# Kernel optimization log

Measured on AMD Instinct MI355X. Metric: run time of the kernel, lower is better.

## Reference

```python
import jax, jax.numpy as jnp
import numpy as np

B, S, D_IN, HID, H, OUT = 4, 2048, 1024, 1024, 16, 128
DH = HID // H
SCALE = float(np.sqrt(DH))
ELEV, FLOOR2 = 4, 32


def setup_inputs() -> dict:
    key = jax.random.key(0)
    ks = jax.random.split(key, 12)
    w = lambda k, o, i: jax.random.normal(k, (o, i), dtype=jnp.float32) * 0.02
    b = lambda k, o: jax.random.normal(k, (o,), dtype=jnp.float32) * 0.02
    return {
        "query": jax.random.normal(ks[0], (B, S, D_IN), dtype=jnp.float32),
        "key": jax.random.normal(ks[1], (B, S, D_IN), dtype=jnp.float32),
        "value": jax.random.normal(ks[2], (B, S, D_IN), dtype=jnp.float32),
        "mask": jax.random.randint(ks[3], (B, 1, 1, S), 0, 2, dtype=jnp.int32),
        "wq_w": w(ks[4], HID, D_IN), "wq_b": b(ks[5], HID),
        "wk_w": w(ks[6], HID, D_IN), "wk_b": b(ks[7], HID),
        "wv_w": w(ks[8], HID, D_IN), "wv_b": b(ks[9], HID),
        "fc_w": w(ks[10], OUT, HID), "fc_b": b(ks[11], OUT),
    }


def reference(query, key, value, mask, wq_w, wq_b, wk_w, wk_b, wv_w, wv_b, fc_w, fc_b):
    bsz, seq = query.shape[0], query.shape[1]
    # torch Linear: x @ W.T + b
    split = lambda x: x.reshape(bsz, seq, H, DH).transpose(0, 2, 1, 3)  # (b,h,s,dh)
    Q = split(query @ wq_w.T + wq_b)
    K = split(key @ wk_w.T + wk_b)
    V = split(value @ wv_w.T + wv_b)
    energy = jnp.einsum('bhqd,bhkd->bhqk', Q, K) / SCALE
    energy = jnp.where(mask == 0, jnp.float32(-1e10), energy)
    attn = jax.nn.softmax(energy, axis=-1)  # dropout is identity in eval mode
    x = jnp.einsum('bhqk,bhkd->bhqd', attn, V)
    x = x.transpose(0, 2, 1, 3).reshape(bsz, seq, HID)
    x = x @ fc_w.T + fc_b
    x = x.reshape(-1, ELEV, FLOOR2)  # (b*s, elevator_num, floor_num*2)
    return jax.nn.softmax(x, axis=1)  # nn.Softmax(dim=1)
```

## Files before the change

### kernel.cpp

```cpp
#include <hip/hip_runtime.h>
#include <stdint.h>

#define S_LEN 2048
#define DK 1024
#define NH 16
#define DH 64
#define LOG2E 1.4426950408889634f
#define M_FIX 10.0f

typedef __attribute__((ext_vector_type(8))) short bf16x8;
typedef __attribute__((ext_vector_type(4))) float f32x4;

__device__ __forceinline__ unsigned short f2bf(float f) {
    union { float f; uint32_t u; } v; v.f = f;
    return (unsigned short)((v.u + 0x7fffu + ((v.u >> 16) & 1u)) >> 16);
}

__device__ __forceinline__ float fast_exp2(float x) {
#if __has_builtin(__builtin_amdgcn_exp2f)
    return __builtin_amdgcn_exp2f(x);
#else
    return exp2f(x);
#endif
}

__device__ __forceinline__ uint32_t cvt_pk_bf16(float a, float b) {
    uint32_t r;
    asm("v_cvt_pk_bf16_f32 %0, %1, %2" : "=v"(r) : "v"(a), "v"(b));
    return r;
}

__device__ __forceinline__ void gload_lds16(const void* g, void* l) {
    __builtin_amdgcn_global_load_lds((const __attribute__((address_space(1))) void*)g,
                                     (__attribute__((address_space(3))) void*)l, 16, 0, 0);
}

__global__ __launch_bounds__(256) void cvt7_kernel(
    const float* __restrict__ a0, const float* __restrict__ a1, const float* __restrict__ a2,
    const float* __restrict__ a3, const float* __restrict__ a4, const float* __restrict__ a5,
    const float* __restrict__ a6,
    unsigned short* __restrict__ o0, unsigned short* __restrict__ o1, unsigned short* __restrict__ o2,
    unsigned short* __restrict__ o3, unsigned short* __restrict__ o4, unsigned short* __restrict__ o5,
    unsigned short* __restrict__ o6,
    int n4_big, int n4_w, int n4_f)
{
    const int y = blockIdx.y;
    const float* in = (y == 0) ? a0 : (y == 1) ? a1 : (y == 2) ? a2 :
                      (y == 3) ? a3 : (y == 4) ? a4 : (y == 5) ? a5 : a6;
    unsigned short* out = (y == 0) ? o0 : (y == 1) ? o1 : (y == 2) ? o2 :
                          (y == 3) ? o3 : (y == 4) ? o4 : (y == 5) ? o5 : o6;
    const int n4 = (y < 3) ? n4_big : ((y < 6) ? n4_w : n4_f);
    const float4* pin = (const float4*)in;
    ushort4* pout = (ushort4*)out;
    int i = blockIdx.x * blockDim.x + threadIdx.x;
    int stride = gridDim.x * blockDim.x;
    for (; i < n4; i += stride) {
        float4 v = pin[i];
        ushort4 o;
        o.x = f2bf(v.x); o.y = f2bf(v.y); o.z = f2bf(v.z); o.w = f2bf(v.w);
        pout[i] = o;
    }
}

__global__ __launch_bounds__(512) void proj_gemm(
    const unsigned short* __restrict__ Xq, const unsigned short* __restrict__ Xk, const unsigned short* __restrict__ Xv,
    const unsigned short* __restrict__ Wq, const unsigned short* __restrict__ Wk, const unsigned short* __restrict__ Wv,
    const float* __restrict__ bq, const float* __restrict__ bk, const float* __restrict__ bv,
    unsigned short* __restrict__ Qh, unsigned short* __restrict__ Kh, unsigned short* __restrict__ Vt)
{
    const int d = blockIdx.x + (blockIdx.y << 3) + (blockIdx.z << 9);
    const int k = d & 7, s = d >> 3;
    const int nn = s & 7;
    const int mz = ((s >> 3) << 3) + k;
    const int m0 = (mz & 63) * 128;
    const int z = mz >> 6;

    const unsigned short* X = (z == 0) ? Xq : ((z == 1) ? Xk : Xv);
    const unsigned short* W = (z == 0) ? Wq : ((z == 1) ? Wk : Wv);
    const float* bias = (z == 0) ? bq : ((z == 1) ? bk : bv);

    const int n0 = nn * 128;
    const int tid = threadIdx.x;
    const int w = tid >> 6;
    const int l = tid & 63;
    const int wm = w >> 2, wn = w & 3;
    const int g = l >> 4, c = l & 15;

    __shared__ __align__(16) unsigned short As[3][128 * 32];
    __shared__ __align__(16) unsigned short Bs[3][128 * 32];

    f32x4 acc[4][2] = {};

    const int srow = l >> 2;
    const int schunk = (((l & 3) - (l >> 3)) & 3) * 8;

    auto stage = [&](int kk, int buf) {
        int r0 = 16 * w;
        gload_lds16(X + (size_t)(m0 + r0 + srow) * DK + kk + schunk, &As[buf][r0 * 32]);
        gload_lds16(W + (size_t)(n0 + r0 + srow) * DK + kk + schunk, &Bs[buf][r0 * 32]);
    };

    stage(0, 0);
    stage(32, 1);

    int cur = 0;
    for (int step = 0; step < 32; ++step) {
        if (step < 31) asm volatile("s_waitcnt vmcnt(2)" ::: "memory");
        else           asm volatile("s_waitcnt vmcnt(0)" ::: "memory");
        __builtin_amdgcn_s_barrier();
        __builtin_amdgcn_sched_barrier(0);

        if (step < 30) {
            int nb = cur + 2; if (nb >= 3) nb -= 3;
            stage((step + 2) << 5, nb);
        }

        bf16x8 a[4], bb[2];
        const int rchunk = 8 * ((g + (c >> 1)) & 3);
#pragma unroll
        for (int mi = 0; mi < 4; ++mi)
            a[mi] = *(const bf16x8*)&As[cur][(64 * wm + 16 * mi + c) * 32 + rchunk];
#pragma unroll
        for (int nj = 0; nj < 2; ++nj)
            bb[nj] = *(const bf16x8*)&Bs[cur][(32 * wn + 16 * nj + c) * 32 + rchunk];
        __builtin_amdgcn_s_setprio(1);
#pragma unroll
        for (int mi = 0; mi < 4; ++mi)
#pragma unroll
            for (int nj = 0; nj < 2; ++nj)
                acc[mi][nj] = __builtin_amdgcn_mfma_f32_16x16x32_bf16(a[mi], bb[nj], acc[mi][nj], 0, 0, 0);
        __builtin_amdgcn_s_setprio(0);

        ++cur; if (cur == 3) cur = 0;
    }

    const float scale = (z == 0) ? (0.125f * LOG2E) : 1.0f;
#pragma unroll
    for (int mi = 0; mi < 4; ++mi) {
#pragma unroll
        for (int nj = 0; nj < 2; ++nj) {
            int col = n0 + 32 * wn + 16 * nj + c;
            float bval = bias[col];
            int h = col >> 6, dh = col & 63;
            int row0 = m0 + 64 * wm + 16 * mi + 4 * g;
            int b = row0 >> 11, ss = row0 & 2047;
            if (z != 2) {
                unsigned short* Out = (z == 0) ? Qh : Kh;
#pragma unroll
                for (int r = 0; r < 4; ++r) {
                    float v = (acc[mi][nj][r] + bval) * scale;
                    Out[((size_t)(b * NH + h) * S_LEN + (ss + r)) * DH + dh] = f2bf(v);
                }
            } else {
                ushort4 o;
                o.x = f2bf(acc[mi][nj][0] + bval);
                o.y = f2bf(acc[mi][nj][1] + bval);
                o.z = f2bf(acc[mi][nj][2] + bval);
                o.w = f2bf(acc[mi][nj][3] + bval);
                int q = (ss >> 2) & 7;
                int newpos = (ss & ~31) + 8 * (q & 3) + 4 * (q >> 2);
                *(ushort4*)&Vt[((size_t)(b * NH + h) * DH + dh) * S_LEN + newpos] = o;
            }
        }
    }
}

__global__ __launch_bounds__(256, 4) void attn_kernel(
    const unsigned short* __restrict__ Qh, const unsigned short* __restrict__ Kh,
    const unsigned short* __restrict__ Vt, const int* __restrict__ maskI,
    unsigned short* __restrict__ O)
{
    const int id = blockIdx.x + (blockIdx.y << 4);
    const int swzid = (id & 7) * 128 + (id >> 3);
    const int q0 = (swzid & 15) * 128;
    const int bh = swzid >> 4;
    const int b = bh >> 4, h = bh & 15;
    const int tid = threadIdx.x, w = tid >> 6, l = tid & 63;
    const int g = l >> 4, c = l & 15;

    __shared__ __align__(16) unsigned short Ks[2][4096];
    __shared__ __align__(16) unsigned short Vs[2][4096];
    __shared__ __align__(16) float mskA[S_LEN];

    bf16x8 qf[2][2];
    const size_t qbase = (size_t)bh * S_LEN + q0 + 32 * w;
#pragma unroll
    for (int mi = 0; mi < 2; ++mi)
#pragma unroll
        for (int k32 = 0; k32 < 2; ++k32)
            qf[mi][k32] = *(const bf16x8*)&Qh[(qbase + 16 * mi + c) * DH + k32 * 32 + 8 * g];

    f32x4 ao[2][4] = {};
    f32x4 ls[2] = {};
    bf16x8 ones;
#pragma unroll
    for (int j = 0; j < 8; ++j) ones[j] = (short)0x3F80;

    const int kswz = ((l & 7) ^ (l >> 3)) * 8;
    const int vrow = l >> 2;
    const int vsrc = (((l & 3) - (l >> 3)) & 3) * 8;

    auto stageKV = [&](int kv, int buf) {
#pragma unroll
        for (int u = 0; u < 2; ++u) {
            int kvs = kv + 32 * u;
            gload_lds16(Kh + ((size_t)bh * S_LEN + kvs + 8 * w + (l >> 3)) * DH + kswz,
                        &Ks[buf][u * 2048 + w * 512]);
            gload_lds16(Vt + ((size_t)bh * DH + 16 * w + vrow) * S_LEN + kvs + vsrc,
                        &Vs[buf][u * 2048 + w * 512]);
        }
    };

    stageKV(0, 0);
    {
        const int4* mp = (const int4*)(maskI + b * S_LEN);
#pragma unroll
        for (int i = 0; i < 2; ++i) {
            int idx = tid + 256 * i;
            int4 m = mp[idx];
            float4 f;
            f.x = m.x ? (-M_FIX * LOG2E) : -3e38f;
            f.y = m.y ? (-M_FIX * LOG2E) : -3e38f;
            f.z = m.z ? (-M_FIX * LOG2E) : -3e38f;
            f.w = m.w ? (-M_FIX * LOG2E) : -3e38f;
            *(float4*)&mskA[idx * 4] = f;
        }
    }

    for (int t = 0; t < 32; ++t) {
        const int cur = t & 1;
        const int kv0 = t << 6;
        __syncthreads();

        if (t < 31) stageKV(kv0 + 64, cur ^ 1);

#pragma unroll
        for (int u = 0; u < 2; ++u) {
            const int base = u * 2048;
            const int kv0s = kv0 + 32 * u;

            float4 mk0 = *(const float4*)&mskA[kv0s + 4 * g];
            float4 mk1 = *(const float4*)&mskA[kv0s + 16 + 4 * g];
            f32x4 sf[2][2];
            sf[0][0] = f32x4{mk0.x, mk0.y, mk0.z, mk0.w};
            sf[1][0] = sf[0][0];
            sf[0][1] = f32x4{mk1.x, mk1.y, mk1.z, mk1.w};
            sf[1][1] = sf[0][1];

            __builtin_amdgcn_s_setprio(1);
#pragma unroll
            for (int nj = 0; nj < 2; ++nj) {
                int krow = 16 * nj + c;
#pragma unroll
                for (int k32 = 0; k32 < 2; ++k32) {
                    int chunk = (k32 * 4 + g) ^ (krow & 7);
                    bf16x8 kf = *(const bf16x8*)&Ks[cur][base + krow * 64 + chunk * 8];
#pragma unroll
                    for (int mi = 0; mi < 2; ++mi)
                        sf[mi][nj] = __builtin_amdgcn_mfma_f32_16x16x32_bf16(kf, qf[mi][k32], sf[mi][nj], 0, 0, 0);
                }
            }
            __builtin_amdgcn_s_setprio(0);

            bf16x8 pf[2];
#pragma unroll
            for (int mi = 0; mi < 2; ++mi) {
                float e00 = fast_exp2(sf[mi][0][0]);
                float e01 = fast_exp2(sf[mi][0][1]);
                float e02 = fast_exp2(sf[mi][0][2]);
                float e03 = fast_exp2(sf[mi][0][3]);
                float e10 = fast_exp2(sf[mi][1][0]);
                float e11 = fast_exp2(sf[mi][1][1]);
                float e12 = fast_exp2(sf[mi][1][2]);
                float e13 = fast_exp2(sf[mi][1][3]);
                union { uint32_t u2[4]; bf16x8 v; } pu;
                pu.u2[0] = cvt_pk_bf16(e00, e01);
                pu.u2[1] = cvt_pk_bf16(e02, e03);
                pu.u2[2] = cvt_pk_bf16(e10, e11);
                pu.u2[3] = cvt_pk_bf16(e12, e13);
                pf[mi] = pu.v;
            }

            __builtin_amdgcn_s_setprio(1);
#pragma unroll
            for (int nc = 0; nc < 4; ++nc) {
                int row = 16 * nc + c;
                int s16 = (g + (c >> 1)) & 3;
                bf16x8 vf = *(const bf16x8*)&Vs[cur][base + row * 32 + 8 * s16];
#pragma unroll
                for (int mi = 0; mi < 2; ++mi)
                    ao[mi][nc] = __builtin_amdgcn_mfma_f32_16x16x32_bf16(pf[mi], vf, ao[mi][nc], 0, 0, 0);
            }
#pragma unroll
            for (int mi = 0; mi < 2; ++mi)
                ls[mi] = __builtin_amdgcn_mfma_f32_16x16x32_bf16(pf[mi], ones, ls[mi], 0, 0, 0);
            __builtin_amdgcn_s_setprio(0);
        }
    }

#pragma unroll
    for (int mi = 0; mi < 2; ++mi)
#pragma unroll
        for (int r = 0; r < 4; ++r) {
            int s = q0 + 32 * w + 16 * mi + 4 * g + r;
            float inv = 1.0f / ls[mi][r];
#pragma unroll
            for (int nc = 0; nc < 4; ++nc) {
                int dh = 16 * nc + c;
                O[(size_t)(b * S_LEN + s) * 1024 + h * DH + dh] = f2bf(ao[mi][nc][r] * inv);
            }
        }
}

__global__ __launch_bounds__(256) void fc_kernel(
    const unsigned short* __restrict__ O, const unsigned short* __restrict__ Wf,
    const float* __restrict__ bfc, float* __restrict__ out)
{
    const int m0 = blockIdx.x * 64;
    const int tid = threadIdx.x, w = tid >> 6, l = tid & 63;
    const int g = l >> 4, c = l & 15;

    __shared__ __align__(16) unsigned short As[3][64 * 32];
    __shared__ __align__(16) unsigned short Bs[3][128 * 32];

    f32x4 acc[8] = {};

    const int srow = l >> 2;
    const int schunk = (((l & 3) - (l >> 3)) & 3) * 8;

    auto stage = [&](int kk, int buf) {
        gload_lds16(O + (size_t)(m0 + 16 * w + srow) * DK + kk + schunk, &As[buf][16 * w * 32]);
#pragma unroll
        for (int j = 0; j < 2; ++j) {
            int r0 = 32 * w + 16 * j;
            gload_lds16(Wf + (size_t)(r0 + srow) * DK + kk + schunk, &Bs[buf][r0 * 32]);
        }
    };

    stage(0, 0);
    stage(32, 1);

    int cur = 0;
    for (int step = 0; step < 32; ++step) {
        if (step < 31) asm volatile("s_waitcnt vmcnt(3)" ::: "memory");
        else           asm volatile("s_waitcnt vmcnt(0)" ::: "memory");
        __builtin_amdgcn_s_barrier();
        __builtin_amdgcn_sched_barrier(0);

        if (step < 30) {
            int nb = cur + 2; if (nb >= 3) nb -= 3;
            stage((step + 2) << 5, nb);
        }

        const int rchunk = 8 * ((g + (c >> 1)) & 3);
        bf16x8 a = *(const bf16x8*)&As[cur][(16 * w + c) * 32 + rchunk];
        bf16x8 bb[8];
#pragma unroll
        for (int nj = 0; nj < 8; ++nj)
            bb[nj] = *(const bf16x8*)&Bs[cur][(16 * nj + c) * 32 + rchunk];
        __builtin_amdgcn_s_setprio(1);
#pragma unroll
        for (int nj = 0; nj < 8; ++nj)
            acc[nj] = __builtin_amdgcn_mfma_f32_16x16x32_bf16(a, bb[nj], acc[nj], 0, 0, 0);
        __builtin_amdgcn_s_setprio(0);

        ++cur; if (cur == 3) cur = 0;
    }

#pragma unroll
    for (int r = 0; r < 4; ++r) {
        int row = m0 + 16 * w + (l >> 4) * 4 + r;
#pragma unroll
        for (int par = 0; par < 2; ++par) {
            float v[4];
#pragma unroll
            for (int e = 0; e < 4; ++e) {
                int col = 16 * (2 * e + par) + (l & 15);
                v[e] = acc[2 * e + par][r] + bfc[col];
            }
            float mx = fmaxf(fmaxf(v[0], v[1]), fmaxf(v[2], v[3]));
            float ex[4], ssum = 0.f;
#pragma unroll
            for (int e = 0; e < 4; ++e) { ex[e] = fast_exp2((v[e] - mx) * LOG2E); ssum += ex[e]; }
            float inv = 1.0f / ssum;
#pragma unroll
            for (int e = 0; e < 4; ++e) {
                int col = 16 * (2 * e + par) + (l & 15);
                out[(size_t)row * 128 + col] = ex[e] * inv;
            }
        }
    }
}

extern "C" void kernel_launch(void* const* d_in, const int* in_sizes, int n_in,
                              void* d_out, int out_size, void* d_ws, size_t ws_size,
                              hipStream_t stream) {
    (void)in_sizes; (void)n_in; (void)out_size; (void)ws_size;
    const float* q    = (const float*)d_in[0];
    const float* k    = (const float*)d_in[1];
    const float* v    = (const float*)d_in[2];
    const int*   mask = (const int*)d_in[3];
    const float* wq_w = (const float*)d_in[4];
    const float* wq_b = (const float*)d_in[5];
    const float* wk_w = (const float*)d_in[6];
    const float* wk_b = (const float*)d_in[7];
    const float* wv_w = (const float*)d_in[8];
    const float* wv_b = (const float*)d_in[9];
    const float* fc_w = (const float*)d_in[10];
    const float* fc_b = (const float*)d_in[11];

    const size_t NX = (size_t)8192 * 1024;
    const size_t NW = (size_t)1024 * 1024;
    const size_t NF = (size_t)128 * 1024;

    unsigned short* Xq = (unsigned short*)d_ws;
    unsigned short* Xk = Xq + NX;
    unsigned short* Xv = Xk + NX;
    unsigned short* Wq = Xv + NX;
    unsigned short* Wk = Wq + NW;
    unsigned short* Wv = Wk + NW;
    unsigned short* Wf = Wv + NW;
    unsigned short* Qh = Wf + NF;
    unsigned short* Kh = Qh + NX;
    unsigned short* Vt = Kh + NX;
    unsigned short* O  = Xq;

    cvt7_kernel<<<dim3(2048, 7), 256, 0, stream>>>(q, k, v, wq_w, wk_w, wv_w, fc_w,
                                                   Xq, Xk, Xv, Wq, Wk, Wv, Wf,
                                                   (int)(NX / 4), (int)(NW / 4), (int)(NF / 4));

    proj_gemm<<<dim3(8, 64, 3), 512, 0, stream>>>(Xq, Xk, Xv, Wq, Wk, Wv,
                                                  wq_b, wk_b, wv_b, Qh, Kh, Vt);
    attn_kernel<<<dim3(16, 64), 256, 0, stream>>>(Qh, Kh, Vt, mask, O);
    fc_kernel<<<128, 256, 0, stream>>>(O, Wf, fc_b, (float*)d_out);
}
```

Before: 184.4 us.

## Switch QKV projection GEMM to double-buffered BK=64 staging with one barrier per step

Replaces the triple-buffered K=32 pipeline in the QKV projection GEMM with a double-buffered pipeline that stages K=64 per iteration as two 32-wide sub-tiles. Each iteration now does one __syncthreads and two MFMA sub-steps, halving barrier count and loop overhead. In exchange the prefetch distance drops from two stages to one, and the explicit vmcnt waits are replaced by a generic syncthreads. LDS usage rises from 48 KB to 64 KB.

```diff
diff --git a/kernel.cpp b/kernel.cpp
--- a/kernel.cpp
+++ b/kernel.cpp
@@ -86,52 +86,54 @@
     const int wm = w >> 2, wn = w & 3;
     const int g = l >> 4, c = l & 15;
 
-    __shared__ __align__(16) unsigned short As[3][128 * 32];
-    __shared__ __align__(16) unsigned short Bs[3][128 * 32];
+    __shared__ __align__(16) unsigned short As[2][2 * 128 * 32];
+    __shared__ __align__(16) unsigned short Bs[2][2 * 128 * 32];
 
     f32x4 acc[4][2] = {};
 
     const int srow = l >> 2;
     const int schunk = (((l & 3) - (l >> 3)) & 3) * 8;
 
+    const int sub = w >> 2;
+    const int rb = 32 * (w & 3);
+
     auto stage = [&](int kk, int buf) {
-        int r0 = 16 * w;
-        gload_lds16(X + (size_t)(m0 + r0 + srow) * DK + kk + schunk, &As[buf][r0 * 32]);
-        gload_lds16(W + (size_t)(n0 + r0 + srow) * DK + kk + schunk, &Bs[buf][r0 * 32]);
+#pragma unroll
+        for (int i = 0; i < 2; ++i) {
+            int r0 = rb + 16 * i;
+            gload_lds16(X + (size_t)(m0 + r0 + srow) * DK + kk + 32 * sub + schunk,
+                        &As[buf][sub * 4096 + r0 * 32]);
+            gload_lds16(W + (size_t)(n0 + r0 + srow) * DK + kk + 32 * sub + schunk,
+                        &Bs[buf][sub * 4096 + r0 * 32]);
+        }
     };
 
     stage(0, 0);
-    stage(32, 1);
-
-    int cur = 0;
-    for (int step = 0; step < 32; ++step) {
-        if (step < 31) asm volatile("s_waitcnt vmcnt(2)" ::: "memory");
-        else           asm volatile("s_waitcnt vmcnt(0)" ::: "memory");
-        __builtin_amdgcn_s_barrier();
-        __builtin_amdgcn_sched_barrier(0);
-
-        if (step < 30) {
-            int nb = cur + 2; if (nb >= 3) nb -= 3;
-            stage((step + 2) << 5, nb);
-        }
-
-        bf16x8 a[4], bb[2];
+
+    for (int t = 0; t < 16; ++t) {
+        const int buf = t & 1;
+        __syncthreads();
+
+        if (t < 15) stage((t + 1) << 6, buf ^ 1);
+
         const int rchunk = 8 * ((g + (c >> 1)) & 3);
-#pragma unroll
-        for (int mi = 0; mi < 4; ++mi)
-            a[mi] = *(const bf16x8*)&As[cur][(64 * wm + 16 * mi + c) * 32 + rchunk];
-#pragma unroll
-        for (int nj = 0; nj < 2; ++nj)
-            bb[nj] = *(const bf16x8*)&Bs[cur][(32 * wn + 16 * nj + c) * 32 + rchunk];
         __builtin_amdgcn_s_setprio(1);
 #pragma unroll
-        for (int mi = 0; mi < 4; ++mi)
+        for (int k32 = 0; k32 < 2; ++k32) {
+            bf16x8 a[4], bb[2];
+#pragma unroll
+            for (int mi = 0; mi < 4; ++mi)
+                a[mi] = *(const bf16x8*)&As[buf][k32 * 4096 + (64 * wm + 16 * mi + c) * 32 + rchunk];
 #pragma unroll
             for (int nj = 0; nj < 2; ++nj)
-                acc[mi][nj] = __builtin_amdgcn_mfma_f32_16x16x32_bf16(a[mi], bb[nj], acc[mi][nj], 0, 0, 0);
+                bb[nj] = *(const bf16x8*)&Bs[buf][k32 * 4096 + (32 * wn + 16 * nj + c) * 32 + rchunk];
+#pragma unroll
+            for (int mi = 0; mi < 4; ++mi)
+#pragma unroll
+                for (int nj = 0; nj < 2; ++nj)
+                    acc[mi][nj] = __builtin_amdgcn_mfma_f32_16x16x32_bf16(a[mi], bb[nj], acc[mi][nj], 0, 0, 0);
+        }
         __builtin_amdgcn_s_setprio(0);
-
-        ++cur; if (cur == 3) cur = 0;
     }
 
     const float scale = (z == 0) ? (0.125f * LOG2E) : 1.0f;
```

After: 178.6 us. -3.2%, faster.
